# Performance work log

Hardware: AMD Instinct MI355X
Metric: run time of the kernel (lower is better)

Reference implementation:

```python
import jax, jax.numpy as jnp
import numpy as np

B, CQ, CKV, H, W = 8, 192, 192, 128, 128
NUM_HEADS = 6
KERNEL_SIZES = (7, 9, 11)
K_BRANCHES = 3
H_I = NUM_HEADS // K_BRANCHES          # heads per branch = 2
DIM_PROJ = 192
HEAD_DIM = DIM_PROJ // NUM_HEADS       # 32
BRANCH_CH = DIM_PROJ // K_BRANCHES     # 64 channels per branch (H_I * HEAD_DIM)
SCALE = HEAD_DIM ** -0.5


def _na2d_branch(q, k, v, ksize, rpb):
    """Neighborhood attention 2D, dilation=1, clamped window (NATTEN semantics).
    q,k,v: [B, h, H, W, d]; rpb: [h, 2K-1, 2K-1] or None. Returns [B, h, H, W, d]."""
    Bq, h, Hq, Wq, d = q.shape
    K = ksize
    NS = K // 2
    # window start clamped so every query sees exactly K keys per axis
    rows = jnp.clip(jnp.arange(Hq) - NS, 0, Hq - K)[:, None] + jnp.arange(K)  # [H, K]
    cols = jnp.clip(jnp.arange(Wq) - NS, 0, Wq - K)[:, None] + jnp.arange(K)  # [W, K]
    qs = q * SCALE
    # scores: loop over the K row-taps (small fixed kernel), vectorized over everything else
    attn_rows = []
    for ki in range(K):
        kr = k[:, :, rows[:, ki]]          # [B,h,H,W,d]  gather key rows
        kc = kr[:, :, :, cols]             # [B,h,H,W,K,d] gather key cols
        attn_rows.append(jnp.einsum('bhijd,bhijkd->bhijk', qs, kc))
    attn = jnp.stack(attn_rows, axis=4)    # [B,h,H,W,K,K]
    if rpb is not None:
        # bias index = (key_pos - query_pos) + (K-1) on each axis
        rel_r = rows - jnp.arange(Hq)[:, None] + (K - 1)   # [H,K] in [0, 2K-2]
        rel_c = cols - jnp.arange(Wq)[:, None] + (K - 1)   # [W,K]
        bias = rpb[:, rel_r][:, :, :, rel_c]               # [h,H,K,W,K]
        bias = jnp.transpose(bias, (0, 1, 3, 2, 4))        # [h,H,W,K,K]
        attn = attn + bias[None]
    attn = jax.nn.softmax(attn.reshape(Bq, h, Hq, Wq, K * K), axis=-1)
    attn = attn.reshape(Bq, h, Hq, Wq, K, K)
    out = jnp.zeros((Bq, h, Hq, Wq, d), q.dtype)
    for ki in range(K):
        vr = v[:, :, rows[:, ki]]          # [B,h,H,W,d]
        vc = vr[:, :, :, cols]             # [B,h,H,W,K,d]
        out = out + jnp.einsum('bhijk,bhijkd->bhijd', attn[:, :, :, :, ki], vc)
    return out


def setup_inputs() -> dict:
    key = jax.random.key(0)
    ks = jax.random.split(key, 16)
    inp = {
        'x': jax.random.normal(ks[0], (B, CQ, H, W), jnp.float32),
        'context': jax.random.normal(ks[1], (B, CKV, H, W), jnp.float32),
        'Wq': jax.random.normal(ks[2], (CQ, DIM_PROJ), jnp.float32) * 0.02,
        'bq': jax.random.normal(ks[3], (DIM_PROJ,), jnp.float32) * 0.02,
        'Wk': jax.random.normal(ks[4], (CKV, DIM_PROJ), jnp.float32) * 0.02,
        'bk': jax.random.normal(ks[5], (DIM_PROJ,), jnp.float32) * 0.02,
        'Wv': jax.random.normal(ks[6], (CKV, DIM_PROJ), jnp.float32) * 0.02,
        'bv': jax.random.normal(ks[7], (DIM_PROJ,), jnp.float32) * 0.02,
        'Wo': jax.random.normal(ks[8], (DIM_PROJ, CQ), jnp.float32) * 0.02,
        'bo': jax.random.normal(ks[9], (CQ,), jnp.float32) * 0.02,
        'rpb0': jax.random.normal(ks[10], (H_I, 2 * 7 - 1, 2 * 7 - 1), jnp.float32) * 0.02,
        'rpb1': jax.random.normal(ks[11], (H_I, 2 * 9 - 1, 2 * 9 - 1), jnp.float32) * 0.02,
        'rpb2': jax.random.normal(ks[12], (H_I, 2 * 11 - 1, 2 * 11 - 1), jnp.float32) * 0.02,
    }
    return inp


def reference(x, context, Wq, bq, Wk, bk, Wv, bv, Wo, bo, rpb0, rpb1, rpb2):
    rpbs = (rpb0, rpb1, rpb2)
    xc = jnp.transpose(x, (0, 2, 3, 1))        # [B,H,W,Cq]
    ctx = jnp.transpose(context, (0, 2, 3, 1))  # [B,H,W,Ckv]
    q = xc @ Wq + bq                            # [B,H,W,192]
    k = ctx @ Wk + bk
    v = ctx @ Wv + bv
    outs = []
    for i, ksize in enumerate(KERNEL_SIZES):
        sl = slice(i * BRANCH_CH, (i + 1) * BRANCH_CH)
        def to_heads(t):
            return jnp.transpose(
                t[..., sl].reshape(B, H, W, H_I, HEAD_DIM), (0, 3, 1, 2, 4))
        o = _na2d_branch(to_heads(q), to_heads(k), to_heads(v), ksize, rpbs[i])
        outs.append(jnp.transpose(o, (0, 2, 3, 1, 4)).reshape(B, H, W, BRANCH_CH))
    out = jnp.concatenate(outs, axis=-1) @ Wo + bo   # [B,H,W,Cq]
    return jnp.transpose(out, (0, 3, 1, 2))          # [B,Cq,H,W]
```

## Files before the change

kernel.cpp:

```cpp
#include <hip/hip_runtime.h>
#include <hip/hip_fp16.h>

#define HH 128
#define WW 128
#define NPIX (HH*WW)
#define NB 8
#define NHEADS 6
#define HD 32
#define SCALE 0.17677669529663687f

typedef _Float16 h2 __attribute__((ext_vector_type(2)));
typedef __fp16 g2 __attribute__((ext_vector_type(2)));
typedef _Float16 f16x4 __attribute__((ext_vector_type(4)));
typedef _Float16 f16x8 __attribute__((ext_vector_type(8)));
typedef float f4 __attribute__((ext_vector_type(4)));

#define LDK 40
union U4 { g2 p2[2]; f16x4 v4; };

__global__ __launch_bounds__(512) void prep_wt(
    const float* __restrict__ Wq, const float* __restrict__ Wk,
    const float* __restrict__ Wv, _Float16* __restrict__ wt)
{
    int idx = blockIdx.x * 512 + threadIdx.x;
    int mat = idx / 36864, rem = idx % 36864;
    int k = rem / 192, n = rem % 192;
    const float* W = mat == 0 ? Wq : (mat == 1 ? Wk : Wv);
    wt[(size_t)mat * 36864 + (size_t)n * 192 + k] = (_Float16)W[(size_t)k * 192 + n];
}

__global__ __launch_bounds__(512, 2) void proj_mfma(
    const float* __restrict__ x, const float* __restrict__ ctx,
    const _Float16* __restrict__ wt,
    const float* __restrict__ bq, const float* __restrict__ bk, const float* __restrict__ bv,
    _Float16* __restrict__ qh, _Float16* __restrict__ kh, _Float16* __restrict__ vh)
{
    int bid = blockIdx.x;
    int xcd = bid & 7;
    int i = bid >> 3;
    int z, xb;
    if (i < 128) { z = 0; xb = xcd * 128 + i; }
    else { int j = i - 128; z = 1 + (j & 1); xb = xcd * 128 + (j >> 1); }

    const float* A  = (z == 0) ? x : ctx;
    const _Float16* WT = wt + (size_t)z * 36864;
    const float* bias = (z == 0) ? bq : (z == 1 ? bk : bv);
    _Float16* outp = (z == 0) ? qh : (z == 1 ? kh : vh);
    float scale = (z == 0) ? SCALE : 1.f;

    __shared__ _Float16 As[128][LDK];

    int t = threadIdx.x;
    int m0 = xb * 128;
    int b  = m0 / NPIX;
    int p0 = m0 % NPIX;
    const float* Ab = A + (size_t)b * 192 * NPIX + p0;

    int lane = t & 63;
    int wid  = t >> 6;
    int wm = wid & 1;
    int wn = wid >> 1;
    int lq = lane & 15;
    int lk = lane >> 4;

    int cq0 = t >> 7, pp = t & 127;

    float ra[2][8];
    f4 acc[12] = {};

    {
        #pragma unroll
        for (int j = 0; j < 4; j++) ra[0][j]     = Ab[(size_t)(4 * cq0 + j) * NPIX + pp];
        #pragma unroll
        for (int j = 0; j < 4; j++) ra[0][4 + j] = Ab[(size_t)(4 * (cq0 + 4) + j) * NPIX + pp];
    }

    #pragma unroll
    for (int ks = 0; ks < 6; ks++) {
        int cur = ks & 1;
        if (ks) __syncthreads();
        {
            U4 u;
            u.p2[0] = __builtin_amdgcn_cvt_pkrtz(ra[cur][0], ra[cur][1]);
            u.p2[1] = __builtin_amdgcn_cvt_pkrtz(ra[cur][2], ra[cur][3]);
            *(f16x4*)&As[pp][4 * cq0] = u.v4;
            u.p2[0] = __builtin_amdgcn_cvt_pkrtz(ra[cur][4], ra[cur][5]);
            u.p2[1] = __builtin_amdgcn_cvt_pkrtz(ra[cur][6], ra[cur][7]);
            *(f16x4*)&As[pp][4 * (cq0 + 4)] = u.v4;
        }
        if (ks < 5) {
            int k0 = (ks + 1) * 32;
            #pragma unroll
            for (int j = 0; j < 4; j++) ra[cur ^ 1][j]     = Ab[(size_t)(k0 + 4 * cq0 + j) * NPIX + pp];
            #pragma unroll
            for (int j = 0; j < 4; j++) ra[cur ^ 1][4 + j] = Ab[(size_t)(k0 + 4 * (cq0 + 4) + j) * NPIX + pp];
        }
        __syncthreads();

        f16x8 wf[3];
        #pragma unroll
        for (int ni = 0; ni < 3; ni++)
            wf[ni] = *(const f16x8*)&WT[(size_t)(wn * 48 + ni * 16 + lq) * 192 + ks * 32 + lk * 8];
        #pragma unroll
        for (int mi = 0; mi < 4; mi++) {
            f16x8 pfr = *(const f16x8*)&As[wm * 64 + mi * 16 + lq][lk * 8];
            #pragma unroll
            for (int ni = 0; ni < 3; ni++)
                acc[mi * 3 + ni] = __builtin_amdgcn_mfma_f32_16x16x32_f16(wf[ni], pfr, acc[mi * 3 + ni], 0, 0, 0);
        }
    }

    #pragma unroll
    for (int mi = 0; mi < 4; mi++) {
        int p = p0 + wm * 64 + mi * 16 + lq;
        #pragma unroll
        for (int ni = 0; ni < 3; ni++) {
            int n0 = wn * 48 + ni * 16 + lk * 4;
            int g = n0 >> 5, d0 = n0 & 31;
            f4 v = acc[mi * 3 + ni];
            U4 u;
            u.p2[0] = __builtin_amdgcn_cvt_pkrtz((v[0] + bias[n0]) * scale,     (v[1] + bias[n0 + 1]) * scale);
            u.p2[1] = __builtin_amdgcn_cvt_pkrtz((v[2] + bias[n0 + 2]) * scale, (v[3] + bias[n0 + 3]) * scale);
            *(f16x4*)(outp + ((size_t)(b * NHEADS + g) * NPIX + p) * HD + d0) = u.v4;
        }
    }
}

#define KS_ELE 33280
#define NA2D_SMEM 134912

template<int K>
__device__ __forceinline__ void na2d_tile(
    const _Float16* __restrict__ qh, const _Float16* __restrict__ kh,
    const _Float16* __restrict__ vh, const float* __restrict__ rpb,
    _Float16* __restrict__ ah, char* smem, int b, int g_head, int hi, int ty, int tx)
{
    constexpr int NS = K / 2;
    constexpr int RW = 2 * K - 1;
    _Float16* Ks = (_Float16*)smem;
    _Float16* Vt = Ks + KS_ELE;
    float* rpbs = (float*)(smem + 2 * KS_ELE * 2);

    int t = threadIdx.x;
    size_t plane = (size_t)(b * NHEADS + g_head) * NPIX;
    int h0 = ty * 16, w0 = tx * 16;
    int rmin = min(max(h0 - NS, 0), HH - K);
    int rtop = min(max(h0 + 15 - NS, 0), HH - K);
    int rows_n = rtop + K - rmin;
    int cwin0 = min(max(w0 - NS, 0), WW - K);
    int ctop = min(max(w0 + 15 - NS, 0), WW - K);
    int cols_n = ctop + K - cwin0;

    for (int i = t; i < RW * RW; i += 512) rpbs[i] = rpb[(size_t)hi * RW * RW + i];

    int ntask = rows_n * 128;
    for (int idx = t; idx < ntask; idx += 512) {
        int row = idx >> 7;
        int key = (idx >> 2) & 31;
        int dc  = idx & 3;
        f16x8 kv = {0,0,0,0,0,0,0,0};
        f16x8 vvv = {0,0,0,0,0,0,0,0};
        if (key < cols_n) {
            size_t pix = plane + (size_t)(rmin + row) * WW + (cwin0 + key);
            kv = *(const f16x8*)&kh[pix * HD + dc * 8];
            vvv = *(const f16x8*)&vh[pix * HD + dc * 8];
        }
        *(f16x8*)&Ks[row * 1280 + key * LDK + dc * 8] = kv;
        int m = 8 * ((key & 15) >> 2) + 4 * (key >> 4) + (key & 3);
        #pragma unroll
        for (int j = 0; j < 8; j++)
            Vt[row * 1280 + (dc * 8 + j) * LDK + m] = vvv[j];
    }
    __syncthreads();

    int lane = t & 63, wid = t >> 6;
    int lq = lane & 15, lg = lane >> 4;
    int wq = w0 + lq;
    int c0q = min(max(wq - NS, 0), WW - K);
    int klo = c0q - cwin0;
    int shiftc = cwin0 - wq + K - 1;
    f4 zf4 = {0.f, 0.f, 0.f, 0.f};

    #pragma unroll 1
    for (int qi = 0; qi < 2; qi++) {
        int qr = wid * 2 + qi;
        int h = h0 + qr;
        int r0q = min(max(h - NS, 0), HH - K);
        int row_base = r0q - rmin;
        f16x8 qf = *(const f16x8*)&qh[(plane + (size_t)h * WW + w0 + lq) * HD + lg * 8];
        f4 acc0 = zf4, acc1 = zf4;
        float lsum = 0.f;

        #pragma unroll 1
        for (int ki = 0; ki < K; ki++) {
            int row = row_base + ki;
            const _Float16* kbase = &Ks[row * 1280 + lg * 8];
            f16x8 a0 = *(const f16x8*)&kbase[lq * LDK];
            f16x8 a1 = *(const f16x8*)&kbase[(16 + lq) * LDK];
            f4 s0 = __builtin_amdgcn_mfma_f32_16x16x32_f16(a0, qf, zf4, 0, 0, 0);
            f4 s1 = __builtin_amdgcn_mfma_f32_16x16x32_f16(a1, qf, zf4, 0, 0, 0);

            int rel_r = r0q + ki - h + K - 1;
            const float* rrow = rpbs + rel_r * RW;
            float pf[2][4];
            #pragma unroll
            for (int c = 0; c < 2; c++) {
                #pragma unroll
                for (int r = 0; r < 4; r++) {
                    int key_local = c * 16 + 4 * lg + r;
                    int rc = key_local + shiftc;
                    rc = min(max(rc, 0), RW - 1);
                    float biasv = rrow[rc];
                    bool valid = (unsigned)(key_local - klo) < (unsigned)K;
                    float sv = (c ? s1[r] : s0[r]) + biasv;
                    float pv = valid ? __expf(sv) : 0.f;
                    pf[c][r] = pv;
                    lsum += pv;
                }
            }
            union { g2 p[4]; f16x8 v; } P;
            P.p[0] = __builtin_amdgcn_cvt_pkrtz(pf[0][0], pf[0][1]);
            P.p[1] = __builtin_amdgcn_cvt_pkrtz(pf[0][2], pf[0][3]);
            P.p[2] = __builtin_amdgcn_cvt_pkrtz(pf[1][0], pf[1][1]);
            P.p[3] = __builtin_amdgcn_cvt_pkrtz(pf[1][2], pf[1][3]);

            const _Float16* vbase = &Vt[row * 1280 + lg * 8];
            f16x8 b0 = *(const f16x8*)&vbase[lq * LDK];
            f16x8 b1 = *(const f16x8*)&vbase[(16 + lq) * LDK];
            acc0 = __builtin_amdgcn_mfma_f32_16x16x32_f16(P.v, b0, acc0, 0, 0, 0);
            acc1 = __builtin_amdgcn_mfma_f32_16x16x32_f16(P.v, b1, acc1, 0, 0, 0);
        }

        lsum += __shfl_xor(lsum, 16);
        lsum += __shfl_xor(lsum, 32);
        float inv = 1.f / lsum;
        _Float16* obase = ah + (plane + (size_t)h * WW + w0) * HD;
        #pragma unroll
        for (int r = 0; r < 4; r++) {
            float ir = __shfl(inv, 4 * lg + r);
            obase[(4 * lg + r) * HD + lq]      = (_Float16)(acc0[r] * ir);
            obase[(4 * lg + r) * HD + lq + 16] = (_Float16)(acc1[r] * ir);
        }
    }
}

__global__ __launch_bounds__(512) void na2d_mfma(
    const _Float16* __restrict__ qh, const _Float16* __restrict__ kh,
    const _Float16* __restrict__ vh,
    const float* __restrict__ rpb0, const float* __restrict__ rpb1,
    const float* __restrict__ rpb2, _Float16* __restrict__ ah)
{
    extern __shared__ char smem[];
    int bid = blockIdx.x;
    int xcd = bid & 7;
    int i = bid >> 3;
    int phase = i >> 7;
    int j = i & 127;
    int lb = xcd * 128 + j;
    int bz = lb >> 6;
    int tile = lb & 63;
    int b = bz >> 1, hi = bz & 1;
    int ty = tile >> 3, tx = tile & 7;
    if (phase == 0)      na2d_tile<7>(qh, kh, vh, rpb0, ah, smem, b, 0 + hi, hi, ty, tx);
    else if (phase == 1) na2d_tile<9>(qh, kh, vh, rpb1, ah, smem, b, 2 + hi, hi, ty, tx);
    else                 na2d_tile<11>(qh, kh, vh, rpb2, ah, smem, b, 4 + hi, hi, ty, tx);
}

__global__ __launch_bounds__(512) void oproj_mfma(
    const _Float16* __restrict__ ah, const float* __restrict__ Wo,
    const float* __restrict__ bo, float* __restrict__ outp)
{
    __shared__ _Float16 Ws[192][LDK];

    int t = threadIdx.x;
    int m0 = blockIdx.x * 128;
    int b  = m0 / NPIX;
    int p0 = m0 % NPIX;

    int lane = t & 63;
    int wid  = t >> 6;
    int wm = wid & 1;
    int wn = wid >> 1;
    int lr = lane & 15;
    int lk = lane >> 4;

    f4 acc[4][3] = {};

    for (int ks = 0; ks < 6; ks++) {
        int k0 = ks * 32;
        #pragma unroll
        for (int i = 0; i < 12; i++) {
            int s = t + i * 512;
            int c = s / 192, n = s - c * 192;
            Ws[n][c] = (_Float16)Wo[(size_t)(k0 + c) * 192 + n];
        }
        __syncthreads();

        const _Float16* abase = ah + (size_t)(b * NHEADS + ks) * NPIX * HD;
        f16x8 af[4], bf[3];
        #pragma unroll
        for (int mi = 0; mi < 4; mi++)
            af[mi] = *(const f16x8*)&abase[(size_t)(p0 + wm * 64 + mi * 16 + lr) * HD + lk * 8];
        #pragma unroll
        for (int ni = 0; ni < 3; ni++)
            bf[ni] = *(const f16x8*)&Ws[wn * 48 + ni * 16 + lr][lk * 8];
        #pragma unroll
        for (int mi = 0; mi < 4; mi++)
            #pragma unroll
            for (int ni = 0; ni < 3; ni++)
                acc[mi][ni] = __builtin_amdgcn_mfma_f32_16x16x32_f16(af[mi], bf[ni], acc[mi][ni], 0, 0, 0);
        __syncthreads();
    }

    #pragma unroll
    for (int ni = 0; ni < 3; ni++) {
        int n = wn * 48 + ni * 16 + lr;
        float bb = bo[n];
        float* obase = outp + ((size_t)b * 192 + n) * NPIX + p0 + wm * 64;
        #pragma unroll
        for (int mi = 0; mi < 4; mi++) {
            f4 v = acc[mi][ni];
            v[0] += bb; v[1] += bb; v[2] += bb; v[3] += bb;
            *(f4*)&obase[mi * 16 + lk * 4] = v;
        }
    }
}

extern "C" void kernel_launch(void* const* d_in, const int* in_sizes, int n_in,
                              void* d_out, int out_size, void* d_ws, size_t ws_size,
                              hipStream_t stream) {
    const float* x    = (const float*)d_in[0];
    const float* ctx  = (const float*)d_in[1];
    const float* Wq   = (const float*)d_in[2];
    const float* bq   = (const float*)d_in[3];
    const float* Wk   = (const float*)d_in[4];
    const float* bk   = (const float*)d_in[5];
    const float* Wv   = (const float*)d_in[6];
    const float* bv   = (const float*)d_in[7];
    const float* Wo   = (const float*)d_in[8];
    const float* bo   = (const float*)d_in[9];
    const float* rpb0 = (const float*)d_in[10];
    const float* rpb1 = (const float*)d_in[11];
    const float* rpb2 = (const float*)d_in[12];

    size_t N = (size_t)NB * NHEADS * NPIX * HD;
    _Float16* qh = (_Float16*)d_ws;
    _Float16* kh = qh + N;
    _Float16* vh = kh + N;
    _Float16* ah = vh + N;
    _Float16* wt = ah;
    float* outp = (float*)d_out;

    (void)hipFuncSetAttribute((const void*)na2d_mfma,
                              hipFuncAttributeMaxDynamicSharedMemorySize, NA2D_SMEM);

    prep_wt<<<216, 512, 0, stream>>>(Wq, Wk, Wv, wt);
    proj_mfma<<<3072, 512, 0, stream>>>(x, ctx, wt, bq, bk, bv, qh, kh, vh);
    na2d_mfma<<<3072, 512, NA2D_SMEM, stream>>>(qh, kh, vh, rpb0, rpb1, rpb2, ah);
    oproj_mfma<<<1024, 512, 0, stream>>>(ah, Wo, bo, outp);
}
```

Baseline: 280.3 us.

## Pre-transpose Wo to fp16 and load full A tile once in projection

Adds a small prep kernel that converts and transposes Wo to fp16 in workspace (reusing the q buffer, which is no longer needed after attention). The output projection then reads weight fragments straight from global memory, removing the per-block shared-memory staging, its fp32-to-fp16 conversion, and the barriers. The input projection now loads the whole 128x192 activation tile into shared memory up front instead of double-buffering it over k-steps. This drops the per-step syncs but uses more LDS and exposes all load latency before any MFMA work starts.

```diff
diff --git a/kernel.cpp b/kernel.cpp
--- a/kernel.cpp
+++ b/kernel.cpp
@@ -29,6 +29,15 @@
     wt[(size_t)mat * 36864 + (size_t)n * 192 + k] = (_Float16)W[(size_t)k * 192 + n];
 }
 
+__global__ __launch_bounds__(512) void prep_wo(
+    const float* __restrict__ Wo, _Float16* __restrict__ woT)
+{
+    int idx = blockIdx.x * 512 + threadIdx.x;
+    int k = idx / 192, n = idx % 192;
+    woT[(size_t)n * 192 + k] = (_Float16)Wo[(size_t)k * 192 + n];
+}
+
+#define LDA 200
 __global__ __launch_bounds__(512, 2) void proj_mfma(
     const float* __restrict__ x, const float* __restrict__ ctx,
     const _Float16* __restrict__ wt,
@@ -48,7 +57,7 @@
     _Float16* outp = (z == 0) ? qh : (z == 1 ? kh : vh);
     float scale = (z == 0) ? SCALE : 1.f;
 
-    __shared__ _Float16 As[128][LDK];
+    __shared__ _Float16 As[128][LDA];
 
     int t = threadIdx.x;
     int m0 = xb * 128;
@@ -63,47 +72,33 @@
     int lq = lane & 15;
     int lk = lane >> 4;
 
-    int cq0 = t >> 7, pp = t & 127;
-
-    float ra[2][8];
+    {
+        int cq = t >> 7, pp = t & 127;
+        #pragma unroll
+        for (int j = 0; j < 12; j++) {
+            int c0 = cq * 48 + j * 4;
+            float a0 = Ab[(size_t)(c0)     * NPIX + pp];
+            float a1 = Ab[(size_t)(c0 + 1) * NPIX + pp];
+            float a2 = Ab[(size_t)(c0 + 2) * NPIX + pp];
+            float a3 = Ab[(size_t)(c0 + 3) * NPIX + pp];
+            U4 u;
+            u.p2[0] = __builtin_amdgcn_cvt_pkrtz(a0, a1);
+            u.p2[1] = __builtin_amdgcn_cvt_pkrtz(a2, a3);
+            *(f16x4*)&As[pp][c0] = u.v4;
+        }
+    }
+    __syncthreads();
+
     f4 acc[12] = {};
-
-    {
-        #pragma unroll
-        for (int j = 0; j < 4; j++) ra[0][j]     = Ab[(size_t)(4 * cq0 + j) * NPIX + pp];
-        #pragma unroll
-        for (int j = 0; j < 4; j++) ra[0][4 + j] = Ab[(size_t)(4 * (cq0 + 4) + j) * NPIX + pp];
-    }
-
     #pragma unroll
     for (int ks = 0; ks < 6; ks++) {
-        int cur = ks & 1;
-        if (ks) __syncthreads();
-        {
-            U4 u;
-            u.p2[0] = __builtin_amdgcn_cvt_pkrtz(ra[cur][0], ra[cur][1]);
-            u.p2[1] = __builtin_amdgcn_cvt_pkrtz(ra[cur][2], ra[cur][3]);
-            *(f16x4*)&As[pp][4 * cq0] = u.v4;
-            u.p2[0] = __builtin_amdgcn_cvt_pkrtz(ra[cur][4], ra[cur][5]);
-            u.p2[1] = __builtin_amdgcn_cvt_pkrtz(ra[cur][6], ra[cur][7]);
-            *(f16x4*)&As[pp][4 * (cq0 + 4)] = u.v4;
-        }
-        if (ks < 5) {
-            int k0 = (ks + 1) * 32;
-            #pragma unroll
-            for (int j = 0; j < 4; j++) ra[cur ^ 1][j]     = Ab[(size_t)(k0 + 4 * cq0 + j) * NPIX + pp];
-            #pragma unroll
-            for (int j = 0; j < 4; j++) ra[cur ^ 1][4 + j] = Ab[(size_t)(k0 + 4 * (cq0 + 4) + j) * NPIX + pp];
-        }
-        __syncthreads();
-
         f16x8 wf[3];
         #pragma unroll
         for (int ni = 0; ni < 3; ni++)
             wf[ni] = *(const f16x8*)&WT[(size_t)(wn * 48 + ni * 16 + lq) * 192 + ks * 32 + lk * 8];
         #pragma unroll
         for (int mi = 0; mi < 4; mi++) {
-            f16x8 pfr = *(const f16x8*)&As[wm * 64 + mi * 16 + lq][lk * 8];
+            f16x8 pfr = *(const f16x8*)&As[wm * 64 + mi * 16 + lq][ks * 32 + lk * 8];
             #pragma unroll
             for (int ni = 0; ni < 3; ni++)
                 acc[mi * 3 + ni] = __builtin_amdgcn_mfma_f32_16x16x32_f16(wf[ni], pfr, acc[mi * 3 + ni], 0, 0, 0);
@@ -267,11 +262,9 @@
 }
 
 __global__ __launch_bounds__(512) void oproj_mfma(
-    const _Float16* __restrict__ ah, const float* __restrict__ Wo,
+    const _Float16* __restrict__ ah, const _Float16* __restrict__ woT,
     const float* __restrict__ bo, float* __restrict__ outp)
 {
-    __shared__ _Float16 Ws[192][LDK];
-
     int t = threadIdx.x;
     int m0 = blockIdx.x * 128;
     int b  = m0 / NPIX;
@@ -286,16 +279,8 @@
 
     f4 acc[4][3] = {};
 
+    #pragma unroll
     for (int ks = 0; ks < 6; ks++) {
-        int k0 = ks * 32;
-        #pragma unroll
-        for (int i = 0; i < 12; i++) {
-            int s = t + i * 512;
-            int c = s / 192, n = s - c * 192;
-            Ws[n][c] = (_Float16)Wo[(size_t)(k0 + c) * 192 + n];
-        }
-        __syncthreads();
-
         const _Float16* abase = ah + (size_t)(b * NHEADS + ks) * NPIX * HD;
         f16x8 af[4], bf[3];
         #pragma unroll
@@ -303,13 +288,12 @@
             af[mi] = *(const f16x8*)&abase[(size_t)(p0 + wm * 64 + mi * 16 + lr) * HD + lk * 8];
         #pragma unroll
         for (int ni = 0; ni < 3; ni++)
-            bf[ni] = *(const f16x8*)&Ws[wn * 48 + ni * 16 + lr][lk * 8];
+            bf[ni] = *(const f16x8*)&woT[(size_t)(wn * 48 + ni * 16 + lr) * 192 + ks * 32 + lk * 8];
         #pragma unroll
         for (int mi = 0; mi < 4; mi++)
             #pragma unroll
             for (int ni = 0; ni < 3; ni++)
                 acc[mi][ni] = __builtin_amdgcn_mfma_f32_16x16x32_f16(af[mi], bf[ni], acc[mi][ni], 0, 0, 0);
-        __syncthreads();
     }
 
     #pragma unroll
@@ -349,6 +333,7 @@
     _Float16* vh = kh + N;
     _Float16* ah = vh + N;
     _Float16* wt = ah;
+    _Float16* woT = qh;
     float* outp = (float*)d_out;
 
     (void)hipFuncSetAttribute((const void*)na2d_mfma,
@@ -357,5 +342,6 @@
     prep_wt<<<216, 512, 0, stream>>>(Wq, Wk, Wv, wt);
     proj_mfma<<<3072, 512, 0, stream>>>(x, ctx, wt, bq, bk, bv, qh, kh, vh);
     na2d_mfma<<<3072, 512, NA2D_SMEM, stream>>>(qh, kh, vh, rpb0, rpb1, rpb2, ah);
-    oproj_mfma<<<1024, 512, 0, stream>>>(ah, Wo, bo, outp);
-}
+    prep_wo<<<72, 512, 0, stream>>>(Wo, woT);
+    oproj_mfma<<<1024, 512, 0, stream>>>(ah, woT, bo, outp);
+}
```

Result: slower. 289.4 us (+3.3%).
